# Kernel optimization log

Measured on AMD Instinct MI355X. Metric: run time of the kernel, lower is better.

## Reference

```python
import jax, jax.numpy as jnp
import numpy as np

B = 4096      # batch
F = 26        # num sparse features
L = 10        # pooling factor (multi-hot indices per feature)
V = 100000    # rows per embedding table
D = 128       # embedding dim (== dense_arch_layer_sizes[-1])
DENSE_IN = 13
DENSE_SIZES = [512, 256, 128]
OVER_SIZES = [1024, 1024, 512, 256, 1]
OVER_IN = D + (F * (F - 1)) // 2 + F  # 479


def _linear_params(key, dims, prefix):
    out = {}
    ks = jax.random.split(key, len(dims) - 1)
    for i in range(len(dims) - 1):
        fan_in = dims[i]
        out[f"{prefix}W{i}"] = jax.random.normal(ks[i], (dims[i], dims[i + 1]), jnp.float32) / np.sqrt(fan_in)
        out[f"{prefix}b{i}"] = jnp.zeros((dims[i + 1],), jnp.float32)
    return out


def setup_inputs() -> dict:
    key = jax.random.key(0)
    k0, k1, k2, k3, k4 = jax.random.split(key, 5)
    inp = {
        "dense_features": jax.random.normal(k0, (B, DENSE_IN), jnp.float32),
        "indices": jax.random.randint(k1, (B, F, L), 0, V, dtype=jnp.int64),
        "tables": jax.random.normal(k2, (F, V, D), jnp.float32) * 0.01,
    }
    inp.update(_linear_params(k3, [DENSE_IN] + DENSE_SIZES, "d"))
    inp.update(_linear_params(k4, [OVER_IN] + OVER_SIZES, "o"))
    return inp


def _dlrm_forward(dense_features, indices, tables,
                  dW0, db0, dW1, db1, dW2, db2,
                  oW0, ob0, oW1, ob1, oW2, ob2, oW3, ob3, oW4, ob4):
    b = dense_features.shape[0]
    # DenseArch: MLP with relu on every layer
    x = dense_features
    for W, bb in ((dW0, db0), (dW1, db1), (dW2, db2)):
        x = jax.nn.relu(x @ W + bb)
    embedded_dense = x  # [B, D]

    # SparseArch: pooled (sum) embedding lookup per feature -> [B, F, D]
    flat_tables = tables.reshape(F * V, D)
    offs = jnp.arange(F, dtype=indices.dtype) * V
    flat_idx = (indices + offs[None, :, None]).reshape(-1)
    gathered = jnp.take(flat_tables, flat_idx, axis=0).reshape(b, F, L, D)
    embedded_sparse = gathered.sum(axis=2)  # [B, F, D]

    # InteractionArch: bmm + upper-triangular gather
    z = jnp.concatenate([embedded_dense[:, None, :], embedded_sparse], axis=1)  # [B, F+1, D]
    inter = jnp.einsum("bnd,bmd->bnm", z, z)  # [B, F+1, F+1]
    iu0, iu1 = np.triu_indices(F + 1, k=1)
    inter_flat = inter[:, iu0, iu1]  # [B, C(F+1,2)]
    feats = jnp.concatenate([embedded_dense, inter_flat], axis=1)  # [B, OVER_IN]

    # OverArch: relu MLP on layer_sizes[:-1], then plain final Linear
    y = feats
    for W, bb in ((oW0, ob0), (oW1, ob1), (oW2, ob2), (oW3, ob3)):
        y = jax.nn.relu(y @ W + bb)
    logits = y @ oW4 + ob4  # [B, 1]
    return logits


def reference(dense_features, indices, tables,
              dW0, db0, dW1, db1, dW2, db2,
              oW0, ob0, oW1, ob1, oW2, ob2, oW3, ob3, oW4, ob4):
    return _dlrm_forward(dense_features, indices, tables,
                         dW0, db0, dW1, db1, dW2, db2,
                         oW0, ob0, oW1, ob1, oW2, ob2, oW3, ob3, oW4, ob4)
```

## Files before the change

kernel.cpp:

```cpp
#include <hip/hip_runtime.h>

#define B_ 4096
#define F_ 26
#define L_ 10
#define V_ 100000
#define D_ 128

typedef __attribute__((ext_vector_type(8))) short short8;
typedef __attribute__((ext_vector_type(4))) float f32x4;

__device__ inline unsigned pack_split(float f) {
    union { float f; unsigned u; } a; a.f = f;
    unsigned r = (a.u + 0x7FFFu + ((a.u >> 16) & 1u)) >> 16;
    union { unsigned u; float f; } hf; hf.u = r << 16;
    float rem = f - hf.f;
    union { float f; unsigned u; } b; b.f = rem;
    unsigned r2 = (b.u + 0x7FFFu + ((b.u >> 16) & 1u)) >> 16;
    return (r << 16) | (r2 & 0xFFFFu);
}
__device__ inline float unpack_f(unsigned u) {
    union { unsigned u; float f; } h; h.u = u & 0xFFFF0000u;
    union { unsigned u; float f; } l; l.u = u << 16;
    return h.f + l.f;
}

__device__ void prep_tile(const float* __restrict__ W, unsigned* __restrict__ Wt,
                          int K, int N, int Kp, int local)
{
    __shared__ float tile[32][33];
    const int t = threadIdx.x;
    const int tx = t & 31, ty = t >> 5;
    const int nbt = N >> 5;
    const int nb = (local % nbt) << 5, kb = (local / nbt) << 5;
    #pragma unroll
    for (int i = 0; i < 4; ++i) {
        int k = kb + ty + i * 8;
        tile[ty + i * 8][tx] = (k < K) ? W[(size_t)k * N + nb + tx] : 0.f;
    }
    __syncthreads();
    #pragma unroll
    for (int i = 0; i < 4; ++i) {
        int nl = ty + i * 8;
        Wt[(size_t)(nb + nl) * Kp + kb + tx] = pack_split(tile[tx][nl]);
    }
}

__global__ __launch_bounds__(256) void prep_all(
    const float* dW0, const float* dW1, const float* dW2,
    const float* oW0, const float* oW1, const float* oW2, const float* oW3,
    unsigned* dWt0, unsigned* dWt1, unsigned* dWt2,
    unsigned* oWt0, unsigned* oWt1, unsigned* oWt2, unsigned* oWt3,
    const float* dense, unsigned* densep)
{
    const int bid = blockIdx.x;
    if      (bid < 16)   prep_tile(dW0, dWt0, 13,   512,  32,   bid);
    else if (bid < 144)  prep_tile(dW1, dWt1, 512,  256,  512,  bid - 16);
    else if (bid < 176)  prep_tile(dW2, dWt2, 256,  128,  256,  bid - 144);
    else if (bid < 656)  prep_tile(oW0, oWt0, 479,  1024, 480,  bid - 176);
    else if (bid < 1680) prep_tile(oW1, oWt1, 1024, 1024, 1024, bid - 656);
    else if (bid < 2192) prep_tile(oW2, oWt2, 1024, 512,  1024, bid - 1680);
    else if (bid < 2320) prep_tile(oW3, oWt3, 512,  256,  512,  bid - 2192);
    else {
        int g = (bid - 2320) * 256 + threadIdx.x;
        int b = g >> 5, k = g & 31;
        densep[g] = (k < 13) ? pack_split(dense[(size_t)b * 13 + k]) : 0u;
    }
}

__global__ __launch_bounds__(512) void gemm8(
    const unsigned* __restrict__ Ap, const unsigned* __restrict__ Wt,
    const float* __restrict__ bias, unsigned* __restrict__ Cp,
    int N, int Kp)
{
    __shared__ __align__(16) unsigned Au[2][128 * 32];
    __shared__ __align__(16) unsigned Bu[2][128 * 32];

    const int t    = threadIdx.x;
    const int lane = t & 63;
    const int w    = t >> 6;
    const int wm   = w >> 2, wn = w & 3;
    const int m0   = blockIdx.y * 128, n0 = blockIdx.x * 128;

    f32x4 acc[4][2];
    const f32x4 zero = {0.f, 0.f, 0.f, 0.f};
    #pragma unroll
    for (int i = 0; i < 4; ++i)
        #pragma unroll
        for (int j = 0; j < 2; ++j) acc[i][j] = zero;

    const unsigned* Ab = Ap + (size_t)m0 * Kp;
    const unsigned* Bb = Wt + (size_t)n0 * Kp;

    const int g4 = lane >> 4;
    const int rr = lane & 15;

    auto STAGE = [&](int buf, int k0) {
        #pragma unroll
        for (int i = 0; i < 2; ++i) {
            int chunk = t + (i << 9);
            int row = chunk >> 3, ch = chunk & 7;
            int sch = ch ^ (row & 7);
            __builtin_amdgcn_global_load_lds(
                (const __attribute__((address_space(1))) unsigned*)(Ab + (size_t)row * Kp + k0 + (sch << 2)),
                &Au[buf][chunk << 2], 16, 0, 0);
        }
        #pragma unroll
        for (int i = 0; i < 2; ++i) {
            int chunk = t + (i << 9);
            int row = chunk >> 3, ch = chunk & 7;
            int sch = ch ^ (row & 7);
            __builtin_amdgcn_global_load_lds(
                (const __attribute__((address_space(1))) unsigned*)(Bb + (size_t)row * Kp + k0 + (sch << 2)),
                &Bu[buf][chunk << 2], 16, 0, 0);
        }
    };

    auto COMPUTE = [&](int buf) {
        const unsigned* au = Au[buf];
        const unsigned* bu = Bu[buf];
        short8 bh[2], bl[2];
        #pragma unroll
        for (int tj = 0; tj < 2; ++tj) {
            int r = wn * 32 + tj * 16 + rr;
            int c0 = (2 * g4) ^ (r & 7), c1 = (2 * g4 + 1) ^ (r & 7);
            uint4 p = *reinterpret_cast<const uint4*>(&bu[r * 32 + (c0 << 2)]);
            uint4 q = *reinterpret_cast<const uint4*>(&bu[r * 32 + (c1 << 2)]);
            union { short8 s; uint4 u; } H, L;
            H.u.x = __builtin_amdgcn_perm(p.y, p.x, 0x07060302u);
            L.u.x = __builtin_amdgcn_perm(p.y, p.x, 0x05040100u);
            H.u.y = __builtin_amdgcn_perm(p.w, p.z, 0x07060302u);
            L.u.y = __builtin_amdgcn_perm(p.w, p.z, 0x05040100u);
            H.u.z = __builtin_amdgcn_perm(q.y, q.x, 0x07060302u);
            L.u.z = __builtin_amdgcn_perm(q.y, q.x, 0x05040100u);
            H.u.w = __builtin_amdgcn_perm(q.w, q.z, 0x07060302u);
            L.u.w = __builtin_amdgcn_perm(q.w, q.z, 0x05040100u);
            bh[tj] = H.s; bl[tj] = L.s;
        }
        #pragma unroll
        for (int ti = 0; ti < 4; ++ti) {
            int r = wm * 64 + ti * 16 + rr;
            int c0 = (2 * g4) ^ (r & 7), c1 = (2 * g4 + 1) ^ (r & 7);
            uint4 p = *reinterpret_cast<const uint4*>(&au[r * 32 + (c0 << 2)]);
            uint4 q = *reinterpret_cast<const uint4*>(&au[r * 32 + (c1 << 2)]);
            union { short8 s; uint4 u; } H, L;
            H.u.x = __builtin_amdgcn_perm(p.y, p.x, 0x07060302u);
            L.u.x = __builtin_amdgcn_perm(p.y, p.x, 0x05040100u);
            H.u.y = __builtin_amdgcn_perm(p.w, p.z, 0x07060302u);
            L.u.y = __builtin_amdgcn_perm(p.w, p.z, 0x05040100u);
            H.u.z = __builtin_amdgcn_perm(q.y, q.x, 0x07060302u);
            L.u.z = __builtin_amdgcn_perm(q.y, q.x, 0x05040100u);
            H.u.w = __builtin_amdgcn_perm(q.w, q.z, 0x07060302u);
            L.u.w = __builtin_amdgcn_perm(q.w, q.z, 0x05040100u);
            short8 ah = H.s, al = L.s;
            #pragma unroll
            for (int tj = 0; tj < 2; ++tj) {
                f32x4 c = acc[ti][tj];
                c = __builtin_amdgcn_mfma_f32_16x16x32_bf16(ah, bh[tj], c, 0, 0, 0);
                c = __builtin_amdgcn_mfma_f32_16x16x32_bf16(ah, bl[tj], c, 0, 0, 0);
                c = __builtin_amdgcn_mfma_f32_16x16x32_bf16(al, bh[tj], c, 0, 0, 0);
                acc[ti][tj] = c;
            }
        }
    };

    const int nt = Kp >> 5;
    STAGE(0, 0);
    __syncthreads();
    int cur = 0;
    for (int ts = 0; ts < nt - 1; ++ts) {
        STAGE(cur ^ 1, (ts + 1) << 5);
        COMPUTE(cur);
        __syncthreads();
        cur ^= 1;
    }
    COMPUTE(cur);

    #pragma unroll
    for (int ti = 0; ti < 4; ++ti) {
        int row = m0 + wm * 64 + ti * 16 + (g4 << 2);
        #pragma unroll
        for (int tj = 0; tj < 2; ++tj) {
            int col = n0 + wn * 32 + tj * 16 + rr;
            float bv = bias[col];
            #pragma unroll
            for (int r = 0; r < 4; ++r) {
                float v = fmaxf(acc[ti][tj][r] + bv, 0.f);
                Cp[(size_t)(row + r) * N + col] = pack_split(v);
            }
        }
    }
}

__global__ __launch_bounds__(256) void gather_bags(
    const int*   __restrict__ idx_words,
    const float* __restrict__ tables,
    unsigned*    __restrict__ bagp)
{
    __shared__ int sstride;
    const int t    = threadIdx.x;
    const int w    = t >> 6;
    const int lane = t & 63;
    const int g    = blockIdx.x * 4 + w;
    const int s    = g / F_;
    const int f    = g - s * F_;

    if (t == 0) {
        int st = 2;
        for (int ww = 1; ww < 256; ww += 2)
            if (idx_words[ww] != 0) { st = 1; break; }
        sstride = st;
    }
    __syncthreads();
    const int st = sstride;

    const float* tab = tables + (size_t)f * V_ * D_;
    const size_t ibase = (size_t)s * (F_ * L_) + (size_t)f * L_;
    float2 a = {0.f, 0.f};
    #pragma unroll
    for (int l = 0; l < L_; ++l) {
        int v = idx_words[(ibase + l) * st];
        v = v < 0 ? 0 : (v >= V_ ? V_ - 1 : v);
        float2 x = *reinterpret_cast<const float2*>(tab + (size_t)v * D_ + 2 * lane);
        a.x += x.x; a.y += x.y;
    }
    uint2 o;
    o.x = pack_split(a.x);
    o.y = pack_split(a.y);
    *reinterpret_cast<uint2*>(bagp + ((size_t)s * F_ + f) * 128 + 2 * lane) = o;
}

__global__ __launch_bounds__(256) void interact_mfma(
    const unsigned* __restrict__ x2p,
    const unsigned* __restrict__ bagp,
    unsigned*       __restrict__ featsp)
{
    __shared__ unsigned zh[4][32][64];
    __shared__ unsigned zl[4][32][64];

    const int t    = threadIdx.x;
    const int w    = t >> 6;
    const int lane = t & 63;
    const int s    = blockIdx.x * 4 + w;

    uint2 xv = *reinterpret_cast<const uint2*>(x2p + (size_t)s * 128 + 2 * lane);
    *reinterpret_cast<uint2*>(featsp + (size_t)s * 480 + 2 * lane) = xv;
    if (lane == 0) featsp[(size_t)s * 480 + 479] = 0u;
    zh[w][0][lane] = (xv.x >> 16) | (xv.y & 0xFFFF0000u);
    zl[w][0][lane] = (xv.x & 0xFFFFu) | (xv.y << 16);

    for (int f = 0; f < F_; ++f) {
        uint2 u = *reinterpret_cast<const uint2*>(bagp + ((size_t)s * F_ + f) * 128 + 2 * lane);
        int r  = f + 1;
        int dw = (((lane >> 2) ^ (r & 7)) << 2) + (lane & 3);
        zh[w][r][dw] = (u.x >> 16) | (u.y & 0xFFFF0000u);
        zl[w][r][dw] = (u.x & 0xFFFFu) | (u.y << 16);
    }
    __syncthreads();

    const int g4 = lane >> 4;
    const int rr = lane & 15;
    f32x4 acc[2][2];
    const f32x4 zero = {0.f, 0.f, 0.f, 0.f};
    acc[0][0] = zero; acc[0][1] = zero; acc[1][0] = zero; acc[1][1] = zero;

    #pragma unroll
    for (int ks = 0; ks < 4; ++ks) {
        short8 h[2], lo[2];
        #pragma unroll
        for (int mi = 0; mi < 2; ++mi) {
            int r = mi * 16 + rr;
            int c = (ks * 4 + g4) ^ (r & 7);
            h[mi]  = *reinterpret_cast<const short8*>(&zh[w][r][c << 2]);
            lo[mi] = *reinterpret_cast<const short8*>(&zl[w][r][c << 2]);
        }
        #pragma unroll
        for (int mi = 0; mi < 2; ++mi)
            #pragma unroll
            for (int nj = 0; nj < 2; ++nj) {
                f32x4 c = acc[mi][nj];
                c = __builtin_amdgcn_mfma_f32_16x16x32_bf16(h[mi],  h[nj],  c, 0, 0, 0);
                c = __builtin_amdgcn_mfma_f32_16x16x32_bf16(h[mi],  lo[nj], c, 0, 0, 0);
                c = __builtin_amdgcn_mfma_f32_16x16x32_bf16(lo[mi], h[nj],  c, 0, 0, 0);
                acc[mi][nj] = c;
            }
    }

    #pragma unroll
    for (int mi = 0; mi < 2; ++mi) {
        #pragma unroll
        for (int nj = 0; nj < 2; ++nj) {
            #pragma unroll
            for (int r = 0; r < 4; ++r) {
                int i = mi * 16 + g4 * 4 + r;
                int j = nj * 16 + rr;
                if (i < j && j <= 26) {
                    int p = i * 26 - (i * (i - 1)) / 2 + (j - i - 1);
                    featsp[(size_t)s * 480 + 128 + p] = pack_split(acc[mi][nj][r]);
                }
            }
        }
    }
}

__global__ __launch_bounds__(256) void final_dot(
    const unsigned* __restrict__ yp, const float* __restrict__ w,
    const float* __restrict__ bias, float* __restrict__ out)
{
    const int wave = threadIdx.x >> 6;
    const int lane = threadIdx.x & 63;
    const int b = blockIdx.x * 4 + wave;
    uint4 u = *reinterpret_cast<const uint4*>(yp + (size_t)b * 256 + lane * 4);
    float4 wv = *reinterpret_cast<const float4*>(&w[lane * 4]);
    float s = unpack_f(u.x) * wv.x + unpack_f(u.y) * wv.y +
              unpack_f(u.z) * wv.z + unpack_f(u.w) * wv.w;
    #pragma unroll
    for (int off = 32; off; off >>= 1) s += __shfl_xor(s, off);
    if (lane == 0) out[b] = s + bias[0];
}

extern "C" void kernel_launch(void* const* d_in, const int* in_sizes, int n_in,
                              void* d_out, int out_size, void* d_ws, size_t ws_size,
                              hipStream_t stream)
{
    const float* dense   = (const float*)d_in[0];
    const int*   indices = (const int*)  d_in[1];
    const float* tables  = (const float*)d_in[2];
    const float* dW0 = (const float*)d_in[3];  const float* db0 = (const float*)d_in[4];
    const float* dW1 = (const float*)d_in[5];  const float* db1 = (const float*)d_in[6];
    const float* dW2 = (const float*)d_in[7];  const float* db2 = (const float*)d_in[8];
    const float* oW0 = (const float*)d_in[9];  const float* ob0 = (const float*)d_in[10];
    const float* oW1 = (const float*)d_in[11]; const float* ob1 = (const float*)d_in[12];
    const float* oW2 = (const float*)d_in[13]; const float* ob2 = (const float*)d_in[14];
    const float* oW3 = (const float*)d_in[15]; const float* ob3 = (const float*)d_in[16];
    const float* oW4 = (const float*)d_in[17]; const float* ob4 = (const float*)d_in[18];
    float* out = (float*)d_out;

    unsigned* wsu = (unsigned*)d_ws;
    unsigned* dWt0 = wsu + 0;
    unsigned* dWt1 = wsu + 16384;
    unsigned* dWt2 = wsu + 147456;
    unsigned* oWt0 = wsu + 180224;
    unsigned* oWt1 = wsu + 671744;
    unsigned* oWt2 = wsu + 1720320;
    unsigned* oWt3 = wsu + 2244608;
    unsigned* densep = wsu + 2375680;
    unsigned* x2p    = wsu + 2506752;
    unsigned* featsp = wsu + 3031040;
    unsigned* x0p    = wsu + 5000000;
    unsigned* x1p    = wsu + 7097152;
    unsigned* y0p    = wsu + 5000000;
    unsigned* y1p    = wsu + 9194304;
    unsigned* y2p    = wsu + 2506752;
    unsigned* y3p    = wsu + 5000000;
    unsigned* bagp   = wsu + 13500000;

    gather_bags<<<(B_ * F_) / 4, 256, 0, stream>>>(indices, tables, bagp);

    prep_all<<<2832, 256, 0, stream>>>(dW0, dW1, dW2, oW0, oW1, oW2, oW3,
                                       dWt0, dWt1, dWt2, oWt0, oWt1, oWt2, oWt3,
                                       dense, densep);

    gemm8<<<dim3(4, 32), 512, 0, stream>>>(densep, dWt0, db0, x0p, 512, 32);
    gemm8<<<dim3(2, 32), 512, 0, stream>>>(x0p,    dWt1, db1, x1p, 256, 512);
    gemm8<<<dim3(1, 32), 512, 0, stream>>>(x1p,    dWt2, db2, x2p, 128, 256);

    interact_mfma<<<B_ / 4, 256, 0, stream>>>(x2p, bagp, featsp);

    gemm8<<<dim3(8, 32), 512, 0, stream>>>(featsp, oWt0, ob0, y0p, 1024, 480);
    gemm8<<<dim3(8, 32), 512, 0, stream>>>(y0p,    oWt1, ob1, y1p, 1024, 1024);
    gemm8<<<dim3(4, 32), 512, 0, stream>>>(y1p,    oWt2, ob2, y2p, 512, 1024);
    gemm8<<<dim3(2, 32), 512, 0, stream>>>(y2p,    oWt3, ob3, y3p, 256, 512);

    final_dot<<<B_ / 4, 256, 0, stream>>>(y3p, oW4, ob4, out);
}
```

Measured before the change: 287.3 us.

## Split embedding gather across prep and dense-MLP launches to overlap with GEMMs

Removes the standalone gather kernel and distributes the 106496 bag reductions across the weight-prep kernel and the three dense-arch GEMM launches as extra blocks. The memory-bound gather can then fill CUs left idle by the small dense GEMM grids. Stride detection becomes a per-wave ballot. The cost is heavier 512-thread blocks running gather work and a larger LDS footprint per block in the gemm_gather kernel.

Result: slower. 304.0 us (+5.8%).

```diff
diff --git a/kernel.cpp b/kernel.cpp
--- a/kernel.cpp
+++ b/kernel.cpp
@@ -24,6 +24,34 @@
     return h.f + l.f;
 }
 
+__device__ __forceinline__ int detect_stride(const int* __restrict__ iw) {
+    const int lane = threadIdx.x & 63;
+    return __any(iw[1 + 2 * lane] != 0) ? 1 : 2;
+}
+
+__device__ __forceinline__ void gather_pair(
+    const int* __restrict__ idx_words, const float* __restrict__ tables,
+    unsigned* __restrict__ bagp, int pair, int st)
+{
+    const int lane = threadIdx.x & 63;
+    const int s = pair / F_;
+    const int f = pair - s * F_;
+    const float* tab = tables + (size_t)f * V_ * D_;
+    const size_t ibase = (size_t)s * (F_ * L_) + (size_t)f * L_;
+    float2 a = {0.f, 0.f};
+    #pragma unroll
+    for (int l = 0; l < L_; ++l) {
+        int v = idx_words[(ibase + l) * st];
+        v = v < 0 ? 0 : (v >= V_ ? V_ - 1 : v);
+        float2 x = *reinterpret_cast<const float2*>(tab + (size_t)v * D_ + 2 * lane);
+        a.x += x.x; a.y += x.y;
+    }
+    uint2 o;
+    o.x = pack_split(a.x);
+    o.y = pack_split(a.y);
+    *reinterpret_cast<uint2*>(bagp + ((size_t)s * F_ + f) * 128 + 2 * lane) = o;
+}
+
 __device__ void prep_tile(const float* __restrict__ W, unsigned* __restrict__ Wt,
                           int K, int N, int Kp, int local)
 {
@@ -45,12 +73,13 @@
     }
 }
 
-__global__ __launch_bounds__(256) void prep_all(
+__global__ __launch_bounds__(256) void prep_gather(
     const float* dW0, const float* dW1, const float* dW2,
     const float* oW0, const float* oW1, const float* oW2, const float* oW3,
     unsigned* dWt0, unsigned* dWt1, unsigned* dWt2,
     unsigned* oWt0, unsigned* oWt1, unsigned* oWt2, unsigned* oWt3,
-    const float* dense, unsigned* densep)
+    const float* dense, unsigned* densep,
+    const int* idx_words, const float* tables, unsigned* bagp)
 {
     const int bid = blockIdx.x;
     if      (bid < 16)   prep_tile(dW0, dWt0, 13,   512,  32,   bid);
@@ -60,14 +89,19 @@
     else if (bid < 1680) prep_tile(oW1, oWt1, 1024, 1024, 1024, bid - 656);
     else if (bid < 2192) prep_tile(oW2, oWt2, 1024, 512,  1024, bid - 1680);
     else if (bid < 2320) prep_tile(oW3, oWt3, 512,  256,  512,  bid - 2192);
-    else {
+    else if (bid < 2832) {
         int g = (bid - 2320) * 256 + threadIdx.x;
         int b = g >> 5, k = g & 31;
         densep[g] = (k < 13) ? pack_split(dense[(size_t)b * 13 + k]) : 0u;
-    }
-}
-
-__global__ __launch_bounds__(512) void gemm8(
+    } else {
+        int st = detect_stride(idx_words);
+        int pair = (bid - 2832) * 4 + (threadIdx.x >> 6);
+        gather_pair(idx_words, tables, bagp, pair, st);
+    }
+}
+
+__device__ __forceinline__ void gemm8_dev(
+    int bid, int gx,
     const unsigned* __restrict__ Ap, const unsigned* __restrict__ Wt,
     const float* __restrict__ bias, unsigned* __restrict__ Cp,
     int N, int Kp)
@@ -79,7 +113,7 @@
     const int lane = t & 63;
     const int w    = t >> 6;
     const int wm   = w >> 2, wn = w & 3;
-    const int m0   = blockIdx.y * 128, n0 = blockIdx.x * 128;
+    const int m0   = (bid / gx) * 128, n0 = (bid % gx) * 128;
 
     f32x4 acc[4][2];
     const f32x4 zero = {0.f, 0.f, 0.f, 0.f};
@@ -191,42 +225,21 @@
     }
 }
 
-__global__ __launch_bounds__(256) void gather_bags(
-    const int*   __restrict__ idx_words,
-    const float* __restrict__ tables,
-    unsigned*    __restrict__ bagp)
-{
-    __shared__ int sstride;
-    const int t    = threadIdx.x;
-    const int w    = t >> 6;
-    const int lane = t & 63;
-    const int g    = blockIdx.x * 4 + w;
-    const int s    = g / F_;
-    const int f    = g - s * F_;
-
-    if (t == 0) {
-        int st = 2;
-        for (int ww = 1; ww < 256; ww += 2)
-            if (idx_words[ww] != 0) { st = 1; break; }
-        sstride = st;
-    }
-    __syncthreads();
-    const int st = sstride;
-
-    const float* tab = tables + (size_t)f * V_ * D_;
-    const size_t ibase = (size_t)s * (F_ * L_) + (size_t)f * L_;
-    float2 a = {0.f, 0.f};
-    #pragma unroll
-    for (int l = 0; l < L_; ++l) {
-        int v = idx_words[(ibase + l) * st];
-        v = v < 0 ? 0 : (v >= V_ ? V_ - 1 : v);
-        float2 x = *reinterpret_cast<const float2*>(tab + (size_t)v * D_ + 2 * lane);
-        a.x += x.x; a.y += x.y;
-    }
-    uint2 o;
-    o.x = pack_split(a.x);
-    o.y = pack_split(a.y);
-    *reinterpret_cast<uint2*>(bagp + ((size_t)s * F_ + f) * 128 + 2 * lane) = o;
+__global__ __launch_bounds__(512) void gemm_gather(
+    const unsigned* __restrict__ Ap, const unsigned* __restrict__ Wt,
+    const float* __restrict__ bias, unsigned* __restrict__ Cp,
+    int N, int Kp, int gemm_blocks, int gx, int pair_base,
+    const int* __restrict__ idx_words, const float* __restrict__ tables,
+    unsigned* __restrict__ bagp)
+{
+    const int bid = blockIdx.x;
+    if (bid < gemm_blocks) {
+        gemm8_dev(bid, gx, Ap, Wt, bias, Cp, N, Kp);
+    } else {
+        int st = detect_stride(idx_words);
+        int pair = pair_base + (bid - gemm_blocks) * 8 + (threadIdx.x >> 6);
+        gather_pair(idx_words, tables, bagp, pair, st);
+    }
 }
 
 __global__ __launch_bounds__(256) void interact_mfma(
@@ -354,22 +367,28 @@
     unsigned* y3p    = wsu + 5000000;
     unsigned* bagp   = wsu + 13500000;
 
-    gather_bags<<<(B_ * F_) / 4, 256, 0, stream>>>(indices, tables, bagp);
-
-    prep_all<<<2832, 256, 0, stream>>>(dW0, dW1, dW2, oW0, oW1, oW2, oW3,
-                                       dWt0, dWt1, dWt2, oWt0, oWt1, oWt2, oWt3,
-                                       dense, densep);
-
-    gemm8<<<dim3(4, 32), 512, 0, stream>>>(densep, dWt0, db0, x0p, 512, 32);
-    gemm8<<<dim3(2, 32), 512, 0, stream>>>(x0p,    dWt1, db1, x1p, 256, 512);
-    gemm8<<<dim3(1, 32), 512, 0, stream>>>(x1p,    dWt2, db2, x2p, 128, 256);
+    prep_gather<<<2832 + 10240, 256, 0, stream>>>(
+        dW0, dW1, dW2, oW0, oW1, oW2, oW3,
+        dWt0, dWt1, dWt2, oWt0, oWt1, oWt2, oWt3,
+        dense, densep, indices, tables, bagp);
+
+    gemm_gather<<<128 + 3072, 512, 0, stream>>>(densep, dWt0, db0, x0p, 512, 32,
+                                                128, 4, 40960, indices, tables, bagp);
+    gemm_gather<<<64 + 2560, 512, 0, stream>>>(x0p, dWt1, db1, x1p, 256, 512,
+                                               64, 2, 65536, indices, tables, bagp);
+    gemm_gather<<<32 + 2560, 512, 0, stream>>>(x1p, dWt2, db2, x2p, 128, 256,
+                                               32, 1, 86016, indices, tables, bagp);
 
     interact_mfma<<<B_ / 4, 256, 0, stream>>>(x2p, bagp, featsp);
 
-    gemm8<<<dim3(8, 32), 512, 0, stream>>>(featsp, oWt0, ob0, y0p, 1024, 480);
-    gemm8<<<dim3(8, 32), 512, 0, stream>>>(y0p,    oWt1, ob1, y1p, 1024, 1024);
-    gemm8<<<dim3(4, 32), 512, 0, stream>>>(y1p,    oWt2, ob2, y2p, 512, 1024);
-    gemm8<<<dim3(2, 32), 512, 0, stream>>>(y2p,    oWt3, ob3, y3p, 256, 512);
+    gemm_gather<<<256, 512, 0, stream>>>(featsp, oWt0, ob0, y0p, 1024, 480,
+                                         256, 8, 0, indices, tables, bagp);
+    gemm_gather<<<256, 512, 0, stream>>>(y0p, oWt1, ob1, y1p, 1024, 1024,
+                                         256, 8, 0, indices, tables, bagp);
+    gemm_gather<<<128, 512, 0, stream>>>(y1p, oWt2, ob2, y2p, 512, 1024,
+                                         128, 4, 0, indices, tables, bagp);
+    gemm_gather<<<64, 512, 0, stream>>>(y2p, oWt3, ob3, y3p, 256, 512,
+                                        64, 2, 0, indices, tables, bagp);
 
     final_dot<<<B_ / 4, 256, 0, stream>>>(y3p, oW4, ob4, out);
 }
```

## Add 64x128-tile gemm4 kernel for over-arch layers and wave-parallel stride detection

Applied to the files above, without the earlier changes.

Adds a new 256-thread GEMM kernel that uses 64x128 output tiles with double-buffered direct-to-LDS loads and split-bf16 MFMA, and uses it for the four over-arch layers in place of the 512-thread gemm8. Halving the M tile doubles the grid, so more blocks are available to fill the CUs when grids are small. The cost is less data reuse per tile. The gather kernel also replaces its serial single-thread index-stride scan and block barrier with a per-wave __any ballot.

Result: slower. 302.2 us (+5.2%).

```diff
diff --git a/kernel.cpp b/kernel.cpp
--- a/kernel.cpp
+++ b/kernel.cpp
@@ -24,6 +24,32 @@
     return h.f + l.f;
 }
 
+__device__ __forceinline__ int detect_stride(const int* __restrict__ iw) {
+    const int lane = threadIdx.x & 63;
+    return __any(iw[1 + 2 * lane] != 0) ? 1 : 2;
+}
+
+__device__ __forceinline__ void gather_pair(
+    const int* __restrict__ idx_words, const float* __restrict__ tables,
+    unsigned* __restrict__ bagp, int s, int f, int st)
+{
+    const int lane = threadIdx.x & 63;
+    const float* tab = tables + (size_t)f * V_ * D_;
+    const size_t ibase = (size_t)s * (F_ * L_) + (size_t)f * L_;
+    float2 a = {0.f, 0.f};
+    #pragma unroll
+    for (int l = 0; l < L_; ++l) {
+        int v = idx_words[(ibase + l) * st];
+        v = v < 0 ? 0 : (v >= V_ ? V_ - 1 : v);
+        float2 x = *reinterpret_cast<const float2*>(tab + (size_t)v * D_ + 2 * lane);
+        a.x += x.x; a.y += x.y;
+    }
+    uint2 o;
+    o.x = pack_split(a.x);
+    o.y = pack_split(a.y);
+    *reinterpret_cast<uint2*>(bagp + ((size_t)s * F_ + f) * 128 + 2 * lane) = o;
+}
+
 __device__ void prep_tile(const float* __restrict__ W, unsigned* __restrict__ Wt,
                           int K, int N, int Kp, int local)
 {
@@ -43,6 +69,18 @@
         int nl = ty + i * 8;
         Wt[(size_t)(nb + nl) * Kp + kb + tx] = pack_split(tile[tx][nl]);
     }
+}
+
+__global__ __launch_bounds__(256) void gather_bags(
+    const int*   __restrict__ idx_words,
+    const float* __restrict__ tables,
+    unsigned*    __restrict__ bagp)
+{
+    const int g = blockIdx.x * 4 + (threadIdx.x >> 6);
+    const int s = g / F_;
+    const int f = g - s * F_;
+    int st = detect_stride(idx_words);
+    gather_pair(idx_words, tables, bagp, s, f, st);
 }
 
 __global__ __launch_bounds__(256) void prep_all(
@@ -191,42 +229,127 @@
     }
 }
 
-__global__ __launch_bounds__(256) void gather_bags(
-    const int*   __restrict__ idx_words,
-    const float* __restrict__ tables,
-    unsigned*    __restrict__ bagp)
-{
-    __shared__ int sstride;
+__global__ __launch_bounds__(256) void gemm4(
+    const unsigned* __restrict__ Ap, const unsigned* __restrict__ Wt,
+    const float* __restrict__ bias, unsigned* __restrict__ Cp,
+    int N, int Kp)
+{
+    __shared__ __align__(16) unsigned Au[2][64 * 32];
+    __shared__ __align__(16) unsigned Bu[2][128 * 32];
+
     const int t    = threadIdx.x;
-    const int w    = t >> 6;
     const int lane = t & 63;
-    const int g    = blockIdx.x * 4 + w;
-    const int s    = g / F_;
-    const int f    = g - s * F_;
-
-    if (t == 0) {
-        int st = 2;
-        for (int ww = 1; ww < 256; ww += 2)
-            if (idx_words[ww] != 0) { st = 1; break; }
-        sstride = st;
-    }
+    const int wn   = t >> 6;
+    const int m0   = blockIdx.y * 64, n0 = blockIdx.x * 128;
+
+    f32x4 acc[4][2];
+    const f32x4 zero = {0.f, 0.f, 0.f, 0.f};
+    #pragma unroll
+    for (int i = 0; i < 4; ++i)
+        #pragma unroll
+        for (int j = 0; j < 2; ++j) acc[i][j] = zero;
+
+    const unsigned* Ab = Ap + (size_t)m0 * Kp;
+    const unsigned* Bb = Wt + (size_t)n0 * Kp;
+
+    const int g4 = lane >> 4;
+    const int rr = lane & 15;
+
+    auto STAGE = [&](int buf, int k0) {
+        #pragma unroll
+        for (int i = 0; i < 2; ++i) {
+            int chunk = t + (i << 8);
+            int row = chunk >> 3, ch = chunk & 7;
+            int sch = ch ^ (row & 7);
+            __builtin_amdgcn_global_load_lds(
+                (const __attribute__((address_space(1))) unsigned*)(Ab + (size_t)row * Kp + k0 + (sch << 2)),
+                &Au[buf][chunk << 2], 16, 0, 0);
+        }
+        #pragma unroll
+        for (int i = 0; i < 4; ++i) {
+            int chunk = t + (i << 8);
+            int row = chunk >> 3, ch = chunk & 7;
+            int sch = ch ^ (row & 7);
+            __builtin_amdgcn_global_load_lds(
+                (const __attribute__((address_space(1))) unsigned*)(Bb + (size_t)row * Kp + k0 + (sch << 2)),
+                &Bu[buf][chunk << 2], 16, 0, 0);
+        }
+    };
+
+    auto COMPUTE = [&](int buf) {
+        const unsigned* au = Au[buf];
+        const unsigned* bu = Bu[buf];
+        short8 bh[2], bl[2];
+        #pragma unroll
+        for (int tj = 0; tj < 2; ++tj) {
+            int r = wn * 32 + tj * 16 + rr;
+            int c0 = (2 * g4) ^ (r & 7), c1 = (2 * g4 + 1) ^ (r & 7);
+            uint4 p = *reinterpret_cast<const uint4*>(&bu[r * 32 + (c0 << 2)]);
+            uint4 q = *reinterpret_cast<const uint4*>(&bu[r * 32 + (c1 << 2)]);
+            union { short8 s; uint4 u; } H, L;
+            H.u.x = __builtin_amdgcn_perm(p.y, p.x, 0x07060302u);
+            L.u.x = __builtin_amdgcn_perm(p.y, p.x, 0x05040100u);
+            H.u.y = __builtin_amdgcn_perm(p.w, p.z, 0x07060302u);
+            L.u.y = __builtin_amdgcn_perm(p.w, p.z, 0x05040100u);
+            H.u.z = __builtin_amdgcn_perm(q.y, q.x, 0x07060302u);
+            L.u.z = __builtin_amdgcn_perm(q.y, q.x, 0x05040100u);
+            H.u.w = __builtin_amdgcn_perm(q.w, q.z, 0x07060302u);
+            L.u.w = __builtin_amdgcn_perm(q.w, q.z, 0x05040100u);
+            bh[tj] = H.s; bl[tj] = L.s;
+        }
+        #pragma unroll
+        for (int ti = 0; ti < 4; ++ti) {
+            int r = ti * 16 + rr;
+            int c0 = (2 * g4) ^ (r & 7), c1 = (2 * g4 + 1) ^ (r & 7);
+            uint4 p = *reinterpret_cast<const uint4*>(&au[r * 32 + (c0 << 2)]);
+            uint4 q = *reinterpret_cast<const uint4*>(&au[r * 32 + (c1 << 2)]);
+            union { short8 s; uint4 u; } H, L;
+            H.u.x = __builtin_amdgcn_perm(p.y, p.x, 0x07060302u);
+            L.u.x = __builtin_amdgcn_perm(p.y, p.x, 0x05040100u);
+            H.u.y = __builtin_amdgcn_perm(p.w, p.z, 0x07060302u);
+            L.u.y = __builtin_amdgcn_perm(p.w, p.z, 0x05040100u);
+            H.u.z = __builtin_amdgcn_perm(q.y, q.x, 0x07060302u);
+            L.u.z = __builtin_amdgcn_perm(q.y, q.x, 0x05040100u);
+            H.u.w = __builtin_amdgcn_perm(q.w, q.z, 0x07060302u);
+            L.u.w = __builtin_amdgcn_perm(q.w, q.z, 0x05040100u);
+            short8 ah = H.s, al = L.s;
+            #pragma unroll
+            for (int tj = 0; tj < 2; ++tj) {
+                f32x4 c = acc[ti][tj];
+                c = __builtin_amdgcn_mfma_f32_16x16x32_bf16(ah, bh[tj], c, 0, 0, 0);
+                c = __builtin_amdgcn_mfma_f32_16x16x32_bf16(ah, bl[tj], c, 0, 0, 0);
+                c = __builtin_amdgcn_mfma_f32_16x16x32_bf16(al, bh[tj], c, 0, 0, 0);
+                acc[ti][tj] = c;
+            }
+        }
+    };
+
+    const int nt = Kp >> 5;
+    STAGE(0, 0);
     __syncthreads();
-    const int st = sstride;
-
-    const float* tab = tables + (size_t)f * V_ * D_;
-    const size_t ibase = (size_t)s * (F_ * L_) + (size_t)f * L_;
-    float2 a = {0.f, 0.f};
-    #pragma unroll
-    for (int l = 0; l < L_; ++l) {
-        int v = idx_words[(ibase + l) * st];
-        v = v < 0 ? 0 : (v >= V_ ? V_ - 1 : v);
-        float2 x = *reinterpret_cast<const float2*>(tab + (size_t)v * D_ + 2 * lane);
-        a.x += x.x; a.y += x.y;
-    }
-    uint2 o;
-    o.x = pack_split(a.x);
-    o.y = pack_split(a.y);
-    *reinterpret_cast<uint2*>(bagp + ((size_t)s * F_ + f) * 128 + 2 * lane) = o;
+    int cur = 0;
+    for (int ts = 0; ts < nt - 1; ++ts) {
+        STAGE(cur ^ 1, (ts + 1) << 5);
+        COMPUTE(cur);
+        __syncthreads();
+        cur ^= 1;
+    }
+    COMPUTE(cur);
+
+    #pragma unroll
+    for (int ti = 0; ti < 4; ++ti) {
+        int row = m0 + ti * 16 + (g4 << 2);
+        #pragma unroll
+        for (int tj = 0; tj < 2; ++tj) {
+            int col = n0 + wn * 32 + tj * 16 + rr;
+            float bv = bias[col];
+            #pragma unroll
+            for (int r = 0; r < 4; ++r) {
+                float v = fmaxf(acc[ti][tj][r] + bv, 0.f);
+                Cp[(size_t)(row + r) * N + col] = pack_split(v);
+            }
+        }
+    }
 }
 
 __global__ __launch_bounds__(256) void interact_mfma(
@@ -366,10 +489,10 @@
 
     interact_mfma<<<B_ / 4, 256, 0, stream>>>(x2p, bagp, featsp);
 
-    gemm8<<<dim3(8, 32), 512, 0, stream>>>(featsp, oWt0, ob0, y0p, 1024, 480);
-    gemm8<<<dim3(8, 32), 512, 0, stream>>>(y0p,    oWt1, ob1, y1p, 1024, 1024);
-    gemm8<<<dim3(4, 32), 512, 0, stream>>>(y1p,    oWt2, ob2, y2p, 512, 1024);
-    gemm8<<<dim3(2, 32), 512, 0, stream>>>(y2p,    oWt3, ob3, y3p, 256, 512);
+    gemm4<<<dim3(8, 64), 256, 0, stream>>>(featsp, oWt0, ob0, y0p, 1024, 480);
+    gemm4<<<dim3(8, 64), 256, 0, stream>>>(y0p,    oWt1, ob1, y1p, 1024, 1024);
+    gemm4<<<dim3(4, 64), 256, 0, stream>>>(y1p,    oWt2, ob2, y2p, 512, 1024);
+    gemm4<<<dim3(2, 64), 256, 0, stream>>>(y2p,    oWt3, ob3, y3p, 256, 512);
 
     final_dot<<<B_ / 4, 256, 0, stream>>>(y3p, oW4, ob4, out);
 }
```
